# Kernel tuning notes

Measured on AMD Instinct MI355X. Metric: run time of the kernel, lower is better.

Reference implementation:

```python
import jax, jax.numpy as jnp
import numpy as np

B = 4096      # batch (tokens)
D_IN = 1024   # input_size_expert
D_HID = 4096  # hidden_size_expert
D_OUT = 1024  # output_size
E = 8         # num_experts


def setup_inputs() -> dict:
    key = jax.random.key(0)
    ks = jax.random.split(key, 9)
    s = lambda fan_in: 1.0 / np.sqrt(fan_in)
    x_expert = jax.random.normal(ks[0], (B, D_IN), dtype=jnp.float32)
    # per-expert weights stacked on leading E axis
    W1 = jax.random.uniform(ks[1], (E, D_IN, D_HID), jnp.float32, -s(D_IN), s(D_IN))
    b1 = jax.random.uniform(ks[2], (E, D_HID), jnp.float32, -s(D_IN), s(D_IN))
    W2 = jax.random.uniform(ks[3], (E, D_HID, D_OUT), jnp.float32, -s(D_HID), s(D_HID))
    b2 = jax.random.uniform(ks[4], (E, D_OUT), jnp.float32, -s(D_HID), s(D_HID))
    # gating network (input_size_gating = input_size_expert, hidden_size_gating = hidden_size_expert)
    Wg1 = jax.random.uniform(ks[5], (D_IN, D_HID), jnp.float32, -s(D_IN), s(D_IN))
    bg1 = jax.random.uniform(ks[6], (D_HID,), jnp.float32, -s(D_IN), s(D_IN))
    Wg2 = jax.random.uniform(ks[7], (D_HID, E), jnp.float32, -s(D_HID), s(D_HID))
    bg2 = jax.random.uniform(ks[8], (E,), jnp.float32, -s(D_HID), s(D_HID))
    return {"x_expert": x_expert, "W1": W1, "b1": b1, "W2": W2, "b2": b2,
            "Wg1": Wg1, "bg1": bg1, "Wg2": Wg2, "bg2": bg2}


def reference(x_expert, W1, b1, W2, b2, Wg1, bg1, Wg2, bg2):
    # gating: MLP + softmax over experts -> [B, E]
    g = jax.nn.relu(x_expert @ Wg1 + bg1)
    gate = jax.nn.softmax(g @ Wg2 + bg2, axis=1)
    # all experts as one batched GEMM: [B, E, D_HID]
    h = jax.nn.relu(jnp.einsum('bi,eih->beh', x_expert, W1) + b1)
    expert_out = jnp.einsum('beh,eho->beo', h, W2) + b2  # [B, E, D_OUT]
    # gate-weighted sum over experts
    return jnp.einsum('be,beo->bo', gate, expert_out)
```

## Files before the change

### kernel.cpp

```cpp
#include <hip/hip_runtime.h>
#include <stdint.h>

typedef __bf16 bf16;
typedef __attribute__((ext_vector_type(8))) __bf16 bf16x8;
typedef __attribute__((ext_vector_type(4))) float f32x4;
typedef unsigned short u16;
typedef unsigned int u32;

#define B_TOK 4096
#define D_IN  1024
#define D_HID 4096
#define D_OUT 1024
#define NE    8
#define KTOT  (NE * D_HID)

__device__ __forceinline__ u16 f2bf(float f) {
  u32 u = __float_as_uint(f);
  return (u16)((u + 0x7FFFu + ((u >> 16) & 1u)) >> 16);
}
__device__ __forceinline__ u32 pack2(float a, float b) {
  return (u32)f2bf(a) | ((u32)f2bf(b) << 16);
}

__global__ __launch_bounds__(256) void cvt_bf16_kernel(const float* __restrict__ in,
                                                       u32* __restrict__ out, long n) {
  long i = ((long)blockIdx.x * 256 + threadIdx.x) * 8;
  if (i >= n) return;
  const float4* pf = (const float4*)(in + i);
  float4 f0 = pf[0], f1 = pf[1];
  uint4 o = make_uint4(pack2(f0.x, f0.y), pack2(f0.z, f0.w),
                       pack2(f1.x, f1.y), pack2(f1.z, f1.w));
  *(uint4*)(out + i / 2) = o;
}

__global__ __launch_bounds__(256) void transpose_bf16_kernel(const float* __restrict__ in,
                                                             u16* __restrict__ out,
                                                             int R, int C) {
  __shared__ u16 tileT[64][68];
  const size_t bo = (size_t)blockIdx.z * R * C;
  const int c0 = blockIdx.x * 64, r0 = blockIdx.y * 64;
  const int tid = threadIdx.x;
  const int lr = tid >> 4;
  const int lc = (tid & 15) * 4;
#pragma unroll
  for (int p = 0; p < 4; ++p) {
    const int r = p * 16 + lr;
    const float4 v = *(const float4*)(in + bo + (size_t)(r0 + r) * C + c0 + lc);
    tileT[lc + 0][r] = f2bf(v.x);
    tileT[lc + 1][r] = f2bf(v.y);
    tileT[lc + 2][r] = f2bf(v.z);
    tileT[lc + 3][r] = f2bf(v.w);
  }
  __syncthreads();
  const int oc  = tid >> 3;
  const int och = (tid & 7) * 8;
#pragma unroll
  for (int p = 0; p < 2; ++p) {
    const int c = p * 32 + oc;
    bf16x8 v = *(const bf16x8*)(&tileT[c][och]);
    *(bf16x8*)(out + bo + (size_t)(c0 + c) * R + r0 + och) = v;
  }
}

template<int MODE>
__global__ __launch_bounds__(256, 4) void gemm_mfma(
    const bf16* __restrict__ A,
    const bf16* __restrict__ Bt,
    const float* __restrict__ bias,
    const float* __restrict__ gate,
    void* __restrict__ Cptr,
    int K, long ldB, long kOffB, long ldC, int kIters, int eArg)
{
  __shared__ __align__(16) bf16 smem[2 * 128 * 64];
  bf16* As = smem;
  bf16* Bs = smem + 128 * 64;

  const int tid  = threadIdx.x;
  const int wave = tid >> 6;
  const int lane = tid & 63;
  const int quad = lane >> 4;
  const int l16  = lane & 15;

  const int m0 = blockIdx.x * 128;
  const int n0 = blockIdx.y * 128;

  int expert = 0;
  long cColOff = 0;
  const bf16* Bp = Bt;
  const float* biasP = bias;
  if (MODE == 1) {
    if (gridDim.z > 1) { expert = blockIdx.z; cColOff = (long)expert * D_HID; }
    else               { expert = eArg; }
    Bp = Bt + (size_t)expert * D_HID * (size_t)ldB;
    biasP = bias + (size_t)expert * D_HID;
  }
  const long kBase = (MODE == 2) ? (long)blockIdx.z * kIters * 64 : 0;

  const int sRow = lane >> 3;
  const int sCol = ((lane & 7) ^ sRow) * 8;

  f32x4 acc[4][4];
#pragma unroll
  for (int i = 0; i < 4; ++i)
#pragma unroll
    for (int j = 0; j < 4; ++j)
      acc[i][j] = (f32x4){0.f, 0.f, 0.f, 0.f};

  const int wr = (wave >> 1) * 64;
  const int wc = (wave & 1) * 64;

  const bf16* aBase = A  + (size_t)(m0 + wave * 32 + sRow) * K   + kBase + sCol;
  const bf16* bBase = Bp + (size_t)(n0 + wave * 32 + sRow) * ldB + kOffB + kBase + sCol;
  bf16* asDst = As + (wave * 32) * 64;
  bf16* bsDst = Bs + (wave * 32) * 64;

  for (int kk = 0; kk < kIters; ++kk) {
    const long ko = (long)kk * 64;
#pragma unroll
    for (int s = 0; s < 4; ++s) {
      __builtin_amdgcn_global_load_lds(
          (__attribute__((address_space(1))) void*)(aBase + (size_t)(s * 8) * K + ko),
          (__attribute__((address_space(3))) void*)(asDst + s * 8 * 64), 16, 0, 0);
      __builtin_amdgcn_global_load_lds(
          (__attribute__((address_space(1))) void*)(bBase + (size_t)(s * 8) * ldB + ko),
          (__attribute__((address_space(3))) void*)(bsDst + s * 8 * 64), 16, 0, 0);
    }
    __syncthreads();
#pragma unroll
    for (int t = 0; t < 2; ++t) {
      bf16x8 af[4], bfv[4];
      const int sw = (((t << 2) + quad) ^ (l16 & 7)) << 3;
#pragma unroll
      for (int i = 0; i < 4; ++i) {
        af[i]  = *(const bf16x8*)(As + (wr + i * 16 + l16) * 64 + sw);
        bfv[i] = *(const bf16x8*)(Bs + (wc + i * 16 + l16) * 64 + sw);
      }
#pragma unroll
      for (int i = 0; i < 4; ++i)
#pragma unroll
        for (int j = 0; j < 4; ++j)
          acc[i][j] = __builtin_amdgcn_mfma_f32_16x16x32_bf16(af[i], bfv[j], acc[i][j], 0, 0, 0);
    }
    __syncthreads();
  }

  if (MODE <= 1) {
    const int SL = 72;
    u16* slab = (u16*)smem + wave * (16 * SL);
    u16* C = (u16*)Cptr;
    float bv[4];
#pragma unroll
    for (int j = 0; j < 4; ++j) bv[j] = biasP[n0 + wc + j * 16 + l16];
#pragma unroll
    for (int i = 0; i < 4; ++i) {
#pragma unroll
      for (int r = 0; r < 4; ++r) {
        const int lrow = quad * 4 + r;
        float sc = 1.0f;
        if (MODE == 1) sc = gate[(size_t)(m0 + wr + i * 16 + lrow) * NE + expert];
#pragma unroll
        for (int j = 0; j < 4; ++j) {
          float v = fmaxf(acc[i][j][r] + bv[j], 0.0f) * sc;
          slab[lrow * SL + j * 16 + l16] = f2bf(v);
        }
      }
      const int rrow = lane & 15;
      const int c0c  = lane >> 4;
      bf16x8 v0 = *(const bf16x8*)(slab + rrow * SL + c0c * 8);
      bf16x8 v1 = *(const bf16x8*)(slab + rrow * SL + (c0c + 4) * 8);
      u16* orow = C + (size_t)(m0 + wr + i * 16 + rrow) * ldC + cColOff + n0 + wc;
      *(bf16x8*)(orow + c0c * 8)       = v0;
      *(bf16x8*)(orow + (c0c + 4) * 8) = v1;
    }
  } else {
    float* C = (float*)Cptr;
#pragma unroll
    for (int i = 0; i < 4; ++i) {
#pragma unroll
      for (int r = 0; r < 4; ++r) {
        const int row = m0 + wr + i * 16 + quad * 4 + r;
        float* crow = C + (size_t)row * ldC + n0 + wc + l16;
#pragma unroll
        for (int j = 0; j < 4; ++j)
          atomicAdd(crow + j * 16, acc[i][j][r]);
      }
    }
  }
}

__global__ __launch_bounds__(256) void gate_softmax_kernel(const bf16* __restrict__ g,
                                                           const float* __restrict__ Wg2,
                                                           const float* __restrict__ bg2,
                                                           float* __restrict__ gate) {
  const int wave = threadIdx.x >> 6, lane = threadIdx.x & 63;
  const int row = blockIdx.x * 4 + wave;
  const bf16* gr = g + (size_t)row * D_HID;
  float acc[NE];
#pragma unroll
  for (int e = 0; e < NE; ++e) acc[e] = 0.f;
  for (int k = lane; k < D_HID; k += 64) {
    const float gv = (float)gr[k];
    const float* w = Wg2 + (size_t)k * NE;
#pragma unroll
    for (int e = 0; e < NE; ++e) acc[e] += gv * w[e];
  }
#pragma unroll
  for (int e = 0; e < NE; ++e) {
    float v = acc[e];
#pragma unroll
    for (int off = 32; off > 0; off >>= 1) v += __shfl_down(v, off);
    acc[e] = v;
  }
  if (lane == 0) {
    float mx = -3.4e38f;
#pragma unroll
    for (int e = 0; e < NE; ++e) { acc[e] += bg2[e]; mx = fmaxf(mx, acc[e]); }
    float s = 0.f;
#pragma unroll
    for (int e = 0; e < NE; ++e) { acc[e] = __expf(acc[e] - mx); s += acc[e]; }
    const float inv = 1.f / s;
#pragma unroll
    for (int e = 0; e < NE; ++e) gate[(size_t)row * NE + e] = acc[e] * inv;
  }
}

__global__ __launch_bounds__(256) void gate_bias_kernel(const float* __restrict__ gate,
                                                        const float* __restrict__ b2,
                                                        float* __restrict__ out) {
  const int idx = blockIdx.x * 256 + threadIdx.x;
  const int b = idx >> 8;
  const int o = (idx & 255) * 4;
  float4 v = {0.f, 0.f, 0.f, 0.f};
#pragma unroll
  for (int e = 0; e < NE; ++e) {
    const float gv = gate[(size_t)b * NE + e];
    const float4 bb = *(const float4*)(b2 + (size_t)e * D_OUT + o);
    v.x += gv * bb.x; v.y += gv * bb.y; v.z += gv * bb.z; v.w += gv * bb.w;
  }
  *(float4*)(out + (size_t)b * D_OUT + o) = v;
}

extern "C" void kernel_launch(void* const* d_in, const int* in_sizes, int n_in,
                              void* d_out, int out_size, void* d_ws, size_t ws_size,
                              hipStream_t stream) {
  const float* x   = (const float*)d_in[0];
  const float* W1  = (const float*)d_in[1];
  const float* b1  = (const float*)d_in[2];
  const float* W2  = (const float*)d_in[3];
  const float* b2  = (const float*)d_in[4];
  const float* Wg1 = (const float*)d_in[5];
  const float* bg1 = (const float*)d_in[6];
  const float* Wg2 = (const float*)d_in[7];
  const float* bg2 = (const float*)d_in[8];
  float* out = (float*)d_out;

  char* p = (char*)d_ws;
  bf16* xb   = (bf16*)p; p += (size_t)B_TOK * D_IN * 2;
  bf16* Wg1t = (bf16*)p; p += (size_t)D_HID * D_IN * 2;
  bf16* W1t  = (bf16*)p; p += (size_t)NE * D_HID * D_IN * 2;
  bf16* W2t  = (bf16*)p; p += (size_t)D_OUT * KTOT * 2;
  bf16* g    = (bf16*)p; p += (size_t)B_TOK * D_HID * 2;
  float* gate= (float*)p; p += (size_t)B_TOK * NE * 4;
  bf16* hs   = (bf16*)p;
  const size_t fixed = (size_t)(p - (char*)d_ws);
  const bool big = ws_size >= fixed + (size_t)B_TOK * KTOT * 2;

  cvt_bf16_kernel<<<(B_TOK * D_IN / 8 + 255) / 256, 256, 0, stream>>>(x, (u32*)xb, (long)B_TOK * D_IN);
  transpose_bf16_kernel<<<dim3(D_HID / 64, D_IN / 64, 1), 256, 0, stream>>>(Wg1, (u16*)Wg1t, D_IN, D_HID);
  transpose_bf16_kernel<<<dim3(D_HID / 64, D_IN / 64, NE), 256, 0, stream>>>(W1, (u16*)W1t, D_IN, D_HID);
  transpose_bf16_kernel<<<dim3(D_OUT / 64, KTOT / 64, 1), 256, 0, stream>>>(W2, (u16*)W2t, KTOT, D_OUT);
  gemm_mfma<0><<<dim3(32, 32, 1), 256, 0, stream>>>(xb, Wg1t, bg1, nullptr, g,
                                                    D_IN, (long)D_IN, 0L, (long)D_HID, D_IN / 64, 0);
  gate_softmax_kernel<<<B_TOK / 4, 256, 0, stream>>>(g, Wg2, bg2, gate);
  gate_bias_kernel<<<B_TOK * D_OUT / 4 / 256, 256, 0, stream>>>(gate, b2, out);

  if (big) {
    gemm_mfma<1><<<dim3(32, 32, NE), 256, 0, stream>>>(xb, W1t, b1, gate, hs,
                                                       D_IN, (long)D_IN, 0L, (long)KTOT, D_IN / 64, 0);
    gemm_mfma<2><<<dim3(32, 8, 4), 256, 0, stream>>>(hs, W2t, nullptr, nullptr, out,
                                                     KTOT, (long)KTOT, 0L, (long)D_OUT, KTOT / 4 / 64, 0);
  } else {
    for (int e = 0; e < NE; ++e) {
      gemm_mfma<1><<<dim3(32, 32, 1), 256, 0, stream>>>(xb, W1t, b1, gate, hs,
                                                        D_IN, (long)D_IN, 0L, (long)D_HID, D_IN / 64, e);
      gemm_mfma<2><<<dim3(32, 8, 2), 256, 0, stream>>>(hs, W2t, nullptr, nullptr, out,
                                                       D_HID, (long)KTOT, (long)e * D_HID, (long)D_OUT,
                                                       D_HID / 2 / 64, e);
    }
  }
}
```

Measured before the change: 1.032 ms.

## Move GEMMs to 256x256 tiles with 8 waves and double-buffered LDS prefetch

Replaces the 128x128, 4-wave MFMA GEMM with a 256x256-tile, 512-thread kernel. It double-buffers LDS so that global_load_lds for the next K tile is issued while MFMAs run on the current one. The K step is split into four phases with explicit barriers, waitcnts, sched_barriers and setprio to interleave LDS reads with MFMA bursts. The goal is more data reuse per block and hidden load latency. The cost is twice the LDS (128 KB), more accumulators per wave and lower occupancy, plus fewer blocks per launch for the smaller grids.

```diff
diff --git a/kernel.cpp b/kernel.cpp
--- a/kernel.cpp
+++ b/kernel.cpp
@@ -63,7 +63,7 @@
 }
 
 template<int MODE>
-__global__ __launch_bounds__(256, 4) void gemm_mfma(
+__global__ __launch_bounds__(512, 2) void gemm_mfma256(
     const bf16* __restrict__ A,
     const bf16* __restrict__ Bt,
     const float* __restrict__ bias,
@@ -71,18 +71,18 @@
     void* __restrict__ Cptr,
     int K, long ldB, long kOffB, long ldC, int kIters, int eArg)
 {
-  __shared__ __align__(16) bf16 smem[2 * 128 * 64];
-  bf16* As = smem;
-  bf16* Bs = smem + 128 * 64;
+  __shared__ __align__(16) bf16 smem[65536];
 
   const int tid  = threadIdx.x;
   const int wave = tid >> 6;
   const int lane = tid & 63;
   const int quad = lane >> 4;
   const int l16  = lane & 15;
-
-  const int m0 = blockIdx.x * 128;
-  const int n0 = blockIdx.y * 128;
+  const int wr = (wave >> 2) * 128;
+  const int wc = (wave & 3) * 64;
+
+  const int m0 = blockIdx.x * 256;
+  const int n0 = blockIdx.y * 256;
 
   int expert = 0;
   long cColOff = 0;
@@ -94,55 +94,127 @@
     Bp = Bt + (size_t)expert * D_HID * (size_t)ldB;
     biasP = bias + (size_t)expert * D_HID;
   }
-  const long kBase = (MODE == 2) ? (long)blockIdx.z * kIters * 64 : 0;
+  const int nt = kIters;
+  const long kBase = (MODE == 2) ? (long)blockIdx.z * nt * 64 : 0;
 
   const int sRow = lane >> 3;
   const int sCol = ((lane & 7) ^ sRow) * 8;
 
-  f32x4 acc[4][4];
-#pragma unroll
-  for (int i = 0; i < 4; ++i)
+  const bf16* aSrc = A  + (size_t)(m0 + wave * 8 + sRow) * K   + kBase + sCol;
+  const bf16* bSrc = Bp + (size_t)(n0 + wave * 8 + sRow) * ldB + kOffB + kBase + sCol;
+  const int dOff = (wave * 8) * 64;
+
+  f32x4 acc[8][4];
+#pragma unroll
+  for (int i = 0; i < 8; ++i)
 #pragma unroll
     for (int j = 0; j < 4; ++j)
       acc[i][j] = (f32x4){0.f, 0.f, 0.f, 0.f};
 
-  const int wr = (wave >> 1) * 64;
-  const int wc = (wave & 1) * 64;
-
-  const bf16* aBase = A  + (size_t)(m0 + wave * 32 + sRow) * K   + kBase + sCol;
-  const bf16* bBase = Bp + (size_t)(n0 + wave * 32 + sRow) * ldB + kOffB + kBase + sCol;
-  bf16* asDst = As + (wave * 32) * 64;
-  bf16* bsDst = Bs + (wave * 32) * 64;
-
-  for (int kk = 0; kk < kIters; ++kk) {
-    const long ko = (long)kk * 64;
-#pragma unroll
-    for (int s = 0; s < 4; ++s) {
-      __builtin_amdgcn_global_load_lds(
-          (__attribute__((address_space(1))) void*)(aBase + (size_t)(s * 8) * K + ko),
-          (__attribute__((address_space(3))) void*)(asDst + s * 8 * 64), 16, 0, 0);
-      __builtin_amdgcn_global_load_lds(
-          (__attribute__((address_space(1))) void*)(bBase + (size_t)(s * 8) * ldB + ko),
-          (__attribute__((address_space(3))) void*)(bsDst + s * 8 * 64), 16, 0, 0);
+#define GLLA(tt, bb) do { \
+    bf16* dstA = smem + (bb) * 32768 + dOff; \
+    const bf16* srcA = aSrc + (size_t)(tt) * 64; \
+    for (int g = 0; g < 4; ++g) \
+      __builtin_amdgcn_global_load_lds( \
+          (__attribute__((address_space(1))) void*)(srcA + (size_t)g * 64 * K), \
+          (__attribute__((address_space(3))) void*)(dstA + g * 64 * 64), 16, 0, 0); \
+  } while (0)
+#define GLLB(tt, bb) do { \
+    bf16* dstB = smem + (bb) * 32768 + 16384 + dOff; \
+    const bf16* srcB = bSrc + (size_t)(tt) * 64; \
+    for (int g = 0; g < 4; ++g) \
+      __builtin_amdgcn_global_load_lds( \
+          (__attribute__((address_space(1))) void*)(srcB + (size_t)g * 64 * ldB), \
+          (__attribute__((address_space(3))) void*)(dstB + g * 64 * 64), 16, 0, 0); \
+  } while (0)
+
+  GLLA(0, 0);
+  GLLB(0, 0);
+
+  for (int t = 0; t < nt; ++t) {
+    const int b = t & 1;
+    const bf16* As_ = smem + b * 32768;
+    const bf16* Bs_ = As_ + 16384;
+    const int swA = ((quad) ^ (l16 & 7)) << 3;
+    const int swB = ((4 + quad) ^ (l16 & 7)) << 3;
+    bf16x8 bfr[4], af[4];
+
+    if (t + 1 < nt) {
+      GLLA(t + 1, b ^ 1);
+      asm volatile("s_waitcnt vmcnt(4)");
+    } else {
+      asm volatile("s_waitcnt vmcnt(0)");
     }
-    __syncthreads();
-#pragma unroll
-    for (int t = 0; t < 2; ++t) {
-      bf16x8 af[4], bfv[4];
-      const int sw = (((t << 2) + quad) ^ (l16 & 7)) << 3;
-#pragma unroll
-      for (int i = 0; i < 4; ++i) {
-        af[i]  = *(const bf16x8*)(As + (wr + i * 16 + l16) * 64 + sw);
-        bfv[i] = *(const bf16x8*)(Bs + (wc + i * 16 + l16) * 64 + sw);
-      }
-#pragma unroll
-      for (int i = 0; i < 4; ++i)
-#pragma unroll
-        for (int j = 0; j < 4; ++j)
-          acc[i][j] = __builtin_amdgcn_mfma_f32_16x16x32_bf16(af[i], bfv[j], acc[i][j], 0, 0, 0);
-    }
-    __syncthreads();
-  }
+    __builtin_amdgcn_s_barrier();
+    __builtin_amdgcn_sched_barrier(0);
+#pragma unroll
+    for (int j = 0; j < 4; ++j)
+      bfr[j] = *(const bf16x8*)(Bs_ + (wc + j * 16 + l16) * 64 + swA);
+#pragma unroll
+    for (int i = 0; i < 4; ++i)
+      af[i] = *(const bf16x8*)(As_ + (wr + i * 16 + l16) * 64 + swA);
+    asm volatile("s_waitcnt lgkmcnt(0)");
+    __builtin_amdgcn_sched_barrier(0);
+    __builtin_amdgcn_s_setprio(1);
+#pragma unroll
+    for (int i = 0; i < 4; ++i)
+#pragma unroll
+      for (int j = 0; j < 4; ++j)
+        acc[i][j] = __builtin_amdgcn_mfma_f32_16x16x32_bf16(af[i], bfr[j], acc[i][j], 0, 0, 0);
+    __builtin_amdgcn_s_setprio(0);
+    __builtin_amdgcn_s_barrier();
+
+#pragma unroll
+    for (int i = 0; i < 4; ++i)
+      af[i] = *(const bf16x8*)(As_ + (wr + 64 + i * 16 + l16) * 64 + swA);
+    if (t + 1 < nt) GLLB(t + 1, b ^ 1);
+    __builtin_amdgcn_s_barrier();
+    asm volatile("s_waitcnt lgkmcnt(0)");
+    __builtin_amdgcn_sched_barrier(0);
+    __builtin_amdgcn_s_setprio(1);
+#pragma unroll
+    for (int i = 0; i < 4; ++i)
+#pragma unroll
+      for (int j = 0; j < 4; ++j)
+        acc[4 + i][j] = __builtin_amdgcn_mfma_f32_16x16x32_bf16(af[i], bfr[j], acc[4 + i][j], 0, 0, 0);
+    __builtin_amdgcn_s_setprio(0);
+    __builtin_amdgcn_s_barrier();
+
+#pragma unroll
+    for (int j = 0; j < 4; ++j)
+      bfr[j] = *(const bf16x8*)(Bs_ + (wc + j * 16 + l16) * 64 + swB);
+#pragma unroll
+    for (int i = 0; i < 4; ++i)
+      af[i] = *(const bf16x8*)(As_ + (wr + i * 16 + l16) * 64 + swB);
+    __builtin_amdgcn_s_barrier();
+    asm volatile("s_waitcnt lgkmcnt(0)");
+    __builtin_amdgcn_sched_barrier(0);
+    __builtin_amdgcn_s_setprio(1);
+#pragma unroll
+    for (int i = 0; i < 4; ++i)
+#pragma unroll
+      for (int j = 0; j < 4; ++j)
+        acc[i][j] = __builtin_amdgcn_mfma_f32_16x16x32_bf16(af[i], bfr[j], acc[i][j], 0, 0, 0);
+    __builtin_amdgcn_s_setprio(0);
+    __builtin_amdgcn_s_barrier();
+
+#pragma unroll
+    for (int i = 0; i < 4; ++i)
+      af[i] = *(const bf16x8*)(As_ + (wr + 64 + i * 16 + l16) * 64 + swB);
+    __builtin_amdgcn_s_barrier();
+    asm volatile("s_waitcnt lgkmcnt(0)");
+    __builtin_amdgcn_sched_barrier(0);
+    __builtin_amdgcn_s_setprio(1);
+#pragma unroll
+    for (int i = 0; i < 4; ++i)
+#pragma unroll
+      for (int j = 0; j < 4; ++j)
+        acc[4 + i][j] = __builtin_amdgcn_mfma_f32_16x16x32_bf16(af[i], bfr[j], acc[4 + i][j], 0, 0, 0);
+    __builtin_amdgcn_s_setprio(0);
+    __builtin_amdgcn_s_barrier();
+  }
+#undef GLLA
+#undef GLLB
 
   if (MODE <= 1) {
     const int SL = 72;
@@ -152,7 +224,7 @@
 #pragma unroll
     for (int j = 0; j < 4; ++j) bv[j] = biasP[n0 + wc + j * 16 + l16];
 #pragma unroll
-    for (int i = 0; i < 4; ++i) {
+    for (int i = 0; i < 8; ++i) {
 #pragma unroll
       for (int r = 0; r < 4; ++r) {
         const int lrow = quad * 4 + r;
@@ -175,7 +247,7 @@
   } else {
     float* C = (float*)Cptr;
 #pragma unroll
-    for (int i = 0; i < 4; ++i) {
+    for (int i = 0; i < 8; ++i) {
 #pragma unroll
       for (int r = 0; r < 4; ++r) {
         const int row = m0 + wr + i * 16 + quad * 4 + r;
@@ -269,23 +341,23 @@
   transpose_bf16_kernel<<<dim3(D_HID / 64, D_IN / 64, 1), 256, 0, stream>>>(Wg1, (u16*)Wg1t, D_IN, D_HID);
   transpose_bf16_kernel<<<dim3(D_HID / 64, D_IN / 64, NE), 256, 0, stream>>>(W1, (u16*)W1t, D_IN, D_HID);
   transpose_bf16_kernel<<<dim3(D_OUT / 64, KTOT / 64, 1), 256, 0, stream>>>(W2, (u16*)W2t, KTOT, D_OUT);
-  gemm_mfma<0><<<dim3(32, 32, 1), 256, 0, stream>>>(xb, Wg1t, bg1, nullptr, g,
-                                                    D_IN, (long)D_IN, 0L, (long)D_HID, D_IN / 64, 0);
+  gemm_mfma256<0><<<dim3(16, 16, 1), 512, 0, stream>>>(xb, Wg1t, bg1, nullptr, g,
+                                                       D_IN, (long)D_IN, 0L, (long)D_HID, D_IN / 64, 0);
   gate_softmax_kernel<<<B_TOK / 4, 256, 0, stream>>>(g, Wg2, bg2, gate);
   gate_bias_kernel<<<B_TOK * D_OUT / 4 / 256, 256, 0, stream>>>(gate, b2, out);
 
   if (big) {
-    gemm_mfma<1><<<dim3(32, 32, NE), 256, 0, stream>>>(xb, W1t, b1, gate, hs,
-                                                       D_IN, (long)D_IN, 0L, (long)KTOT, D_IN / 64, 0);
-    gemm_mfma<2><<<dim3(32, 8, 4), 256, 0, stream>>>(hs, W2t, nullptr, nullptr, out,
-                                                     KTOT, (long)KTOT, 0L, (long)D_OUT, KTOT / 4 / 64, 0);
+    gemm_mfma256<1><<<dim3(16, 16, NE), 512, 0, stream>>>(xb, W1t, b1, gate, hs,
+                                                          D_IN, (long)D_IN, 0L, (long)KTOT, D_IN / 64, 0);
+    gemm_mfma256<2><<<dim3(16, 4, 4), 512, 0, stream>>>(hs, W2t, nullptr, nullptr, out,
+                                                        KTOT, (long)KTOT, 0L, (long)D_OUT, KTOT / 4 / 64, 0);
   } else {
     for (int e = 0; e < NE; ++e) {
-      gemm_mfma<1><<<dim3(32, 32, 1), 256, 0, stream>>>(xb, W1t, b1, gate, hs,
-                                                        D_IN, (long)D_IN, 0L, (long)D_HID, D_IN / 64, e);
-      gemm_mfma<2><<<dim3(32, 8, 2), 256, 0, stream>>>(hs, W2t, nullptr, nullptr, out,
-                                                       D_HID, (long)KTOT, (long)e * D_HID, (long)D_OUT,
-                                                       D_HID / 2 / 64, e);
+      gemm_mfma256<1><<<dim3(16, 16, 1), 512, 0, stream>>>(xb, W1t, b1, gate, hs,
+                                                           D_IN, (long)D_IN, 0L, (long)D_HID, D_IN / 64, e);
+      gemm_mfma256<2><<<dim3(16, 4, 2), 512, 0, stream>>>(hs, W2t, nullptr, nullptr, out,
+                                                          D_HID, (long)KTOT, (long)e * D_HID, (long)D_OUT,
+                                                          D_HID / 2 / 64, e);
     }
   }
 }
```

After: 958.4 us. 7.1% less time.

## Rewrite MFMA GEMM as 256x256 tile, 512-thread kernel with 4-stage LDS pipeline

Applied to the files above, without the earlier changes.

Replaces the 128x128 single-buffered GEMM with a 256x256 tile kernel using 8 waves, each computing a 128x64 sub-tile. K tiles are 32 wide and move through a 4-deep LDS ring via global_load_lds, with loads issued three tiles ahead and explicit vmcnt waits, barriers and setprio around the MFMA bursts. Workgroup IDs are remapped so consecutive tiles are spread across the eight XCDs. The aim is to hide global-memory latency and raise arithmetic intensity per tile. The cost is more registers and LDS, and fewer workgroups, which hurts the small gating and split-K launches.

```diff
diff --git a/kernel.cpp b/kernel.cpp
--- a/kernel.cpp
+++ b/kernel.cpp
@@ -13,6 +13,9 @@
 #define D_OUT 1024
 #define NE    8
 #define KTOT  (NE * D_HID)
+
+#define AS1 __attribute__((address_space(1)))
+#define AS3 __attribute__((address_space(3)))
 
 __device__ __forceinline__ u16 f2bf(float f) {
   u32 u = __float_as_uint(f);
@@ -63,7 +66,7 @@
 }
 
 template<int MODE>
-__global__ __launch_bounds__(256, 4) void gemm_mfma(
+__global__ __launch_bounds__(512, 2) void gemm_mfma256(
     const bf16* __restrict__ A,
     const bf16* __restrict__ Bt,
     const float* __restrict__ bias,
@@ -71,78 +74,125 @@
     void* __restrict__ Cptr,
     int K, long ldB, long kOffB, long ldC, int kIters, int eArg)
 {
-  __shared__ __align__(16) bf16 smem[2 * 128 * 64];
-  bf16* As = smem;
-  bf16* Bs = smem + 128 * 64;
+  __shared__ __align__(16) bf16 smem[65536];
 
   const int tid  = threadIdx.x;
   const int wave = tid >> 6;
   const int lane = tid & 63;
   const int quad = lane >> 4;
   const int l16  = lane & 15;
-
-  const int m0 = blockIdx.x * 128;
-  const int n0 = blockIdx.y * 128;
+  const int wr = (wave >> 2) * 128;
+  const int wc = (wave & 3) * 64;
+
+  const int gx = gridDim.x, gy = gridDim.y;
+  const int nwg = gx * gy * gridDim.z;
+  const int orig = blockIdx.x + gx * (blockIdx.y + gy * blockIdx.z);
+  const int cid = (orig & 7) * (nwg >> 3) + (orig >> 3);
+  const int bx = cid % gx;
+  const int rest = cid / gx;
+  const int by = rest % gy;
+  const int bz = rest / gy;
+
+  const int m0 = bx * 256;
+  const int n0 = by * 256;
 
   int expert = 0;
   long cColOff = 0;
   const bf16* Bp = Bt;
   const float* biasP = bias;
   if (MODE == 1) {
-    if (gridDim.z > 1) { expert = blockIdx.z; cColOff = (long)expert * D_HID; }
+    if (gridDim.z > 1) { expert = bz; cColOff = (long)expert * D_HID; }
     else               { expert = eArg; }
     Bp = Bt + (size_t)expert * D_HID * (size_t)ldB;
     biasP = bias + (size_t)expert * D_HID;
   }
-  const long kBase = (MODE == 2) ? (long)blockIdx.z * kIters * 64 : 0;
-
-  const int sRow = lane >> 3;
-  const int sCol = ((lane & 7) ^ sRow) * 8;
-
-  f32x4 acc[4][4];
-#pragma unroll
-  for (int i = 0; i < 4; ++i)
+  const int nt = kIters;
+  const long kBase = (MODE == 2) ? (long)bz * nt * 32 : 0;
+
+  const int sRow = lane >> 2;
+  const int sCol = ((lane & 3) ^ ((lane >> 3) & 3)) * 8;
+
+  const bf16* aSrc = A  + (size_t)(m0 + wave * 32 + sRow) * K   + kBase + sCol;
+  const bf16* bSrc = Bp + (size_t)(n0 + wave * 32 + sRow) * ldB + kOffB + kBase + sCol;
+
+  const int xorv = (quad ^ ((l16 >> 1) & 3)) * 8;
+  int aOff[8], bOff[4];
+#pragma unroll
+  for (int i = 0; i < 8; ++i) aOff[i] = (wr + i * 16 + l16) * 32 + xorv;
+#pragma unroll
+  for (int j = 0; j < 4; ++j) bOff[j] = (wc + j * 16 + l16) * 32 + xorv;
+
+  f32x4 acc[8][4];
+#pragma unroll
+  for (int i = 0; i < 8; ++i)
 #pragma unroll
     for (int j = 0; j < 4; ++j)
       acc[i][j] = (f32x4){0.f, 0.f, 0.f, 0.f};
 
-  const int wr = (wave >> 1) * 64;
-  const int wc = (wave & 1) * 64;
-
-  const bf16* aBase = A  + (size_t)(m0 + wave * 32 + sRow) * K   + kBase + sCol;
-  const bf16* bBase = Bp + (size_t)(n0 + wave * 32 + sRow) * ldB + kOffB + kBase + sCol;
-  bf16* asDst = As + (wave * 32) * 64;
-  bf16* bsDst = Bs + (wave * 32) * 64;
-
-  for (int kk = 0; kk < kIters; ++kk) {
-    const long ko = (long)kk * 64;
-#pragma unroll
-    for (int s = 0; s < 4; ++s) {
-      __builtin_amdgcn_global_load_lds(
-          (__attribute__((address_space(1))) void*)(aBase + (size_t)(s * 8) * K + ko),
-          (__attribute__((address_space(3))) void*)(asDst + s * 8 * 64), 16, 0, 0);
-      __builtin_amdgcn_global_load_lds(
-          (__attribute__((address_space(1))) void*)(bBase + (size_t)(s * 8) * ldB + ko),
-          (__attribute__((address_space(3))) void*)(bsDst + s * 8 * 64), 16, 0, 0);
-    }
-    __syncthreads();
-#pragma unroll
-    for (int t = 0; t < 2; ++t) {
-      bf16x8 af[4], bfv[4];
-      const int sw = (((t << 2) + quad) ^ (l16 & 7)) << 3;
-#pragma unroll
-      for (int i = 0; i < 4; ++i) {
-        af[i]  = *(const bf16x8*)(As + (wr + i * 16 + l16) * 64 + sw);
-        bfv[i] = *(const bf16x8*)(Bs + (wc + i * 16 + l16) * 64 + sw);
-      }
-#pragma unroll
-      for (int i = 0; i < 4; ++i)
-#pragma unroll
-        for (int j = 0; j < 4; ++j)
-          acc[i][j] = __builtin_amdgcn_mfma_f32_16x16x32_bf16(af[i], bfv[j], acc[i][j], 0, 0, 0);
-    }
-    __syncthreads();
-  }
+#define GLLA(tt, bb) do { \
+    bf16* d_ = smem + (bb) * 16384 + wave * 1024; \
+    const bf16* s_ = aSrc + (size_t)(tt) * 32; \
+    __builtin_amdgcn_global_load_lds((AS1 void*)(s_), (AS3 void*)(d_), 16, 0, 0); \
+    __builtin_amdgcn_global_load_lds((AS1 void*)(s_ + (size_t)16 * K), (AS3 void*)(d_ + 512), 16, 0, 0); \
+  } while (0)
+#define GLLB(tt, bb) do { \
+    bf16* d_ = smem + (bb) * 16384 + 8192 + wave * 1024; \
+    const bf16* s_ = bSrc + (size_t)(tt) * 32; \
+    __builtin_amdgcn_global_load_lds((AS1 void*)(s_), (AS3 void*)(d_), 16, 0, 0); \
+    __builtin_amdgcn_global_load_lds((AS1 void*)(s_ + (size_t)16 * ldB), (AS3 void*)(d_ + 512), 16, 0, 0); \
+  } while (0)
+
+#define TILE_BODY(T, VMW, ISS) do { \
+    const bf16* Ab_ = smem + ((T) & 3) * 16384; \
+    const bf16* Bb_ = Ab_ + 8192; \
+    bf16x8 af_[4], bf_[4]; \
+    if (ISS) GLLA((T) + 3, ((T) + 3) & 3); \
+    asm volatile("s_waitcnt vmcnt(" #VMW ")"); \
+    __builtin_amdgcn_s_barrier(); \
+    __builtin_amdgcn_sched_barrier(0); \
+    _Pragma("unroll") \
+    for (int j_ = 0; j_ < 4; ++j_) bf_[j_] = *(const bf16x8*)(Bb_ + bOff[j_]); \
+    _Pragma("unroll") \
+    for (int i_ = 0; i_ < 4; ++i_) af_[i_] = *(const bf16x8*)(Ab_ + aOff[i_]); \
+    asm volatile("s_waitcnt lgkmcnt(0)"); \
+    __builtin_amdgcn_sched_barrier(0); \
+    __builtin_amdgcn_s_setprio(1); \
+    _Pragma("unroll") \
+    for (int i_ = 0; i_ < 4; ++i_) \
+      _Pragma("unroll") \
+      for (int j_ = 0; j_ < 4; ++j_) \
+        acc[i_][j_] = __builtin_amdgcn_mfma_f32_16x16x32_bf16(af_[i_], bf_[j_], acc[i_][j_], 0, 0, 0); \
+    __builtin_amdgcn_s_setprio(0); \
+    __builtin_amdgcn_s_barrier(); \
+    _Pragma("unroll") \
+    for (int i_ = 0; i_ < 4; ++i_) af_[i_] = *(const bf16x8*)(Ab_ + aOff[4 + i_]); \
+    if (ISS) GLLB((T) + 3, ((T) + 3) & 3); \
+    __builtin_amdgcn_s_barrier(); \
+    asm volatile("s_waitcnt lgkmcnt(0)"); \
+    __builtin_amdgcn_sched_barrier(0); \
+    __builtin_amdgcn_s_setprio(1); \
+    _Pragma("unroll") \
+    for (int i_ = 0; i_ < 4; ++i_) \
+      _Pragma("unroll") \
+      for (int j_ = 0; j_ < 4; ++j_) \
+        acc[4 + i_][j_] = __builtin_amdgcn_mfma_f32_16x16x32_bf16(af_[i_], bf_[j_], acc[4 + i_][j_], 0, 0, 0); \
+    __builtin_amdgcn_s_setprio(0); \
+    __builtin_amdgcn_s_barrier(); \
+  } while (0)
+
+  GLLA(0, 0); GLLB(0, 0);
+  GLLA(1, 1); GLLB(1, 1);
+  GLLA(2, 2); GLLB(2, 2);
+
+  int t = 0;
+  for (; t < nt - 3; ++t) TILE_BODY(t, 10, 1);
+  TILE_BODY(t, 8, 0); ++t;
+  TILE_BODY(t, 4, 0); ++t;
+  TILE_BODY(t, 0, 0);
+
+#undef GLLA
+#undef GLLB
+#undef TILE_BODY
 
   if (MODE <= 1) {
     const int SL = 72;
@@ -152,7 +202,7 @@
 #pragma unroll
     for (int j = 0; j < 4; ++j) bv[j] = biasP[n0 + wc + j * 16 + l16];
 #pragma unroll
-    for (int i = 0; i < 4; ++i) {
+    for (int i = 0; i < 8; ++i) {
 #pragma unroll
       for (int r = 0; r < 4; ++r) {
         const int lrow = quad * 4 + r;
@@ -175,7 +225,7 @@
   } else {
     float* C = (float*)Cptr;
 #pragma unroll
-    for (int i = 0; i < 4; ++i) {
+    for (int i = 0; i < 8; ++i) {
 #pragma unroll
       for (int r = 0; r < 4; ++r) {
         const int row = m0 + wr + i * 16 + quad * 4 + r;
@@ -269,23 +319,23 @@
   transpose_bf16_kernel<<<dim3(D_HID / 64, D_IN / 64, 1), 256, 0, stream>>>(Wg1, (u16*)Wg1t, D_IN, D_HID);
   transpose_bf16_kernel<<<dim3(D_HID / 64, D_IN / 64, NE), 256, 0, stream>>>(W1, (u16*)W1t, D_IN, D_HID);
   transpose_bf16_kernel<<<dim3(D_OUT / 64, KTOT / 64, 1), 256, 0, stream>>>(W2, (u16*)W2t, KTOT, D_OUT);
-  gemm_mfma<0><<<dim3(32, 32, 1), 256, 0, stream>>>(xb, Wg1t, bg1, nullptr, g,
-                                                    D_IN, (long)D_IN, 0L, (long)D_HID, D_IN / 64, 0);
+  gemm_mfma256<0><<<dim3(16, 16, 1), 512, 0, stream>>>(xb, Wg1t, bg1, nullptr, g,
+                                                       D_IN, (long)D_IN, 0L, (long)D_HID, D_IN / 32, 0);
   gate_softmax_kernel<<<B_TOK / 4, 256, 0, stream>>>(g, Wg2, bg2, gate);
   gate_bias_kernel<<<B_TOK * D_OUT / 4 / 256, 256, 0, stream>>>(gate, b2, out);
 
   if (big) {
-    gemm_mfma<1><<<dim3(32, 32, NE), 256, 0, stream>>>(xb, W1t, b1, gate, hs,
-                                                       D_IN, (long)D_IN, 0L, (long)KTOT, D_IN / 64, 0);
-    gemm_mfma<2><<<dim3(32, 8, 4), 256, 0, stream>>>(hs, W2t, nullptr, nullptr, out,
-                                                     KTOT, (long)KTOT, 0L, (long)D_OUT, KTOT / 4 / 64, 0);
+    gemm_mfma256<1><<<dim3(16, 16, NE), 512, 0, stream>>>(xb, W1t, b1, gate, hs,
+                                                          D_IN, (long)D_IN, 0L, (long)KTOT, D_IN / 32, 0);
+    gemm_mfma256<2><<<dim3(16, 4, 4), 512, 0, stream>>>(hs, W2t, nullptr, nullptr, out,
+                                                        KTOT, (long)KTOT, 0L, (long)D_OUT, KTOT / 4 / 32, 0);
   } else {
     for (int e = 0; e < NE; ++e) {
-      gemm_mfma<1><<<dim3(32, 32, 1), 256, 0, stream>>>(xb, W1t, b1, gate, hs,
-                                                        D_IN, (long)D_IN, 0L, (long)D_HID, D_IN / 64, e);
-      gemm_mfma<2><<<dim3(32, 8, 2), 256, 0, stream>>>(hs, W2t, nullptr, nullptr, out,
-                                                       D_HID, (long)KTOT, (long)e * D_HID, (long)D_OUT,
-                                                       D_HID / 2 / 64, e);
+      gemm_mfma256<1><<<dim3(16, 16, 1), 512, 0, stream>>>(xb, W1t, b1, gate, hs,
+                                                           D_IN, (long)D_IN, 0L, (long)D_HID, D_IN / 32, e);
+      gemm_mfma256<2><<<dim3(16, 4, 2), 512, 0, stream>>>(hs, W2t, nullptr, nullptr, out,
+                                                          D_HID, (long)KTOT, (long)e * D_HID, (long)D_OUT,
+                                                          D_HID / 2 / 32, e);
     }
   }
 }
```

Result: slower. 1.087 ms (+5.3%).

## Switch GEMMs to 256x256 tiles with 8 waves and double-buffered LDS loads

Applied to the files above, without the earlier changes.

Replaces the 128x128, 4-wave GEMM with a 256x256-tile, 512-thread kernel. Each wave now computes a 128x64 sub-tile with 8x4 MFMA accumulators. LDS is double-buffered so the next K tile's global-to-LDS load overlaps the current tile's MFMAs, with one barrier per iteration, and s_setprio raises wave priority around the MFMA block. The aim is more data reuse per byte loaded and less sync stall. The cost is much higher register and LDS use (128KB smem), fewer blocks in flight, and a smaller grid for the gating GEMM.

```diff
diff --git a/kernel.cpp b/kernel.cpp
--- a/kernel.cpp
+++ b/kernel.cpp
@@ -13,6 +13,9 @@
 #define D_OUT 1024
 #define NE    8
 #define KTOT  (NE * D_HID)
+
+#define AS1 __attribute__((address_space(1)))
+#define AS3 __attribute__((address_space(3)))
 
 __device__ __forceinline__ u16 f2bf(float f) {
   u32 u = __float_as_uint(f);
@@ -63,7 +66,7 @@
 }
 
 template<int MODE>
-__global__ __launch_bounds__(256, 4) void gemm_mfma(
+__global__ __launch_bounds__(512, 2) void gemm_mfma256(
     const bf16* __restrict__ A,
     const bf16* __restrict__ Bt,
     const float* __restrict__ bias,
@@ -71,18 +74,18 @@
     void* __restrict__ Cptr,
     int K, long ldB, long kOffB, long ldC, int kIters, int eArg)
 {
-  __shared__ __align__(16) bf16 smem[2 * 128 * 64];
-  bf16* As = smem;
-  bf16* Bs = smem + 128 * 64;
+  __shared__ __align__(16) bf16 smem[65536];
 
   const int tid  = threadIdx.x;
   const int wave = tid >> 6;
   const int lane = tid & 63;
   const int quad = lane >> 4;
   const int l16  = lane & 15;
-
-  const int m0 = blockIdx.x * 128;
-  const int n0 = blockIdx.y * 128;
+  const int wr = (wave >> 2) * 128;
+  const int wc = (wave & 3) * 64;
+
+  const int m0 = blockIdx.x * 256;
+  const int n0 = blockIdx.y * 256;
 
   int expert = 0;
   long cColOff = 0;
@@ -94,55 +97,65 @@
     Bp = Bt + (size_t)expert * D_HID * (size_t)ldB;
     biasP = bias + (size_t)expert * D_HID;
   }
-  const long kBase = (MODE == 2) ? (long)blockIdx.z * kIters * 64 : 0;
+  const int nt = kIters;
+  const long kBase = (MODE == 2) ? (long)blockIdx.z * nt * 64 : 0;
 
   const int sRow = lane >> 3;
   const int sCol = ((lane & 7) ^ sRow) * 8;
 
-  f32x4 acc[4][4];
-#pragma unroll
-  for (int i = 0; i < 4; ++i)
+  const bf16* aSrc = A  + (size_t)(m0 + wave * 8 + sRow) * K   + kBase + sCol;
+  const bf16* bSrc = Bp + (size_t)(n0 + wave * 8 + sRow) * ldB + kOffB + kBase + sCol;
+  const int dOff = (wave * 8) * 64;
+
+  f32x4 acc[8][4];
+#pragma unroll
+  for (int i = 0; i < 8; ++i)
 #pragma unroll
     for (int j = 0; j < 4; ++j)
       acc[i][j] = (f32x4){0.f, 0.f, 0.f, 0.f};
 
-  const int wr = (wave >> 1) * 64;
-  const int wc = (wave & 1) * 64;
-
-  const bf16* aBase = A  + (size_t)(m0 + wave * 32 + sRow) * K   + kBase + sCol;
-  const bf16* bBase = Bp + (size_t)(n0 + wave * 32 + sRow) * ldB + kOffB + kBase + sCol;
-  bf16* asDst = As + (wave * 32) * 64;
-  bf16* bsDst = Bs + (wave * 32) * 64;
-
-  for (int kk = 0; kk < kIters; ++kk) {
-    const long ko = (long)kk * 64;
-#pragma unroll
-    for (int s = 0; s < 4; ++s) {
-      __builtin_amdgcn_global_load_lds(
-          (__attribute__((address_space(1))) void*)(aBase + (size_t)(s * 8) * K + ko),
-          (__attribute__((address_space(3))) void*)(asDst + s * 8 * 64), 16, 0, 0);
-      __builtin_amdgcn_global_load_lds(
-          (__attribute__((address_space(1))) void*)(bBase + (size_t)(s * 8) * ldB + ko),
-          (__attribute__((address_space(3))) void*)(bsDst + s * 8 * 64), 16, 0, 0);
+#define GLL(tt, bb) do { \
+    bf16* dstA = smem + (bb) * 32768 + dOff; \
+    bf16* dstB = dstA + 16384; \
+    const bf16* srcA = aSrc + (size_t)(tt) * 64; \
+    const bf16* srcB = bSrc + (size_t)(tt) * 64; \
+    _Pragma("unroll") \
+    for (int g_ = 0; g_ < 4; ++g_) { \
+      __builtin_amdgcn_global_load_lds((AS1 void*)(srcA + (size_t)g_ * 64 * K), \
+                                       (AS3 void*)(dstA + g_ * 64 * 64), 16, 0, 0); \
+      __builtin_amdgcn_global_load_lds((AS1 void*)(srcB + (size_t)g_ * 64 * ldB), \
+                                       (AS3 void*)(dstB + g_ * 64 * 64), 16, 0, 0); \
+    } \
+  } while (0)
+
+  GLL(0, 0);
+
+  for (int t = 0; t < nt; ++t) {
+    const bf16* Ab = smem + (t & 1) * 32768;
+    const bf16* Bb = Ab + 16384;
+    asm volatile("s_waitcnt vmcnt(0)" ::: "memory");
+    __builtin_amdgcn_s_barrier();
+    if (t + 1 < nt) GLL(t + 1, (t + 1) & 1);
+#pragma unroll
+    for (int kh = 0; kh < 2; ++kh) {
+      const int sw = (((kh << 2) + quad) ^ (l16 & 7)) << 3;
+      bf16x8 bv[4], av[8];
+#pragma unroll
+      for (int j = 0; j < 4; ++j)
+        bv[j] = *(const bf16x8*)(Bb + (wc + j * 16 + l16) * 64 + sw);
+#pragma unroll
+      for (int i = 0; i < 8; ++i)
+        av[i] = *(const bf16x8*)(Ab + (wr + i * 16 + l16) * 64 + sw);
+      __builtin_amdgcn_s_setprio(1);
+#pragma unroll
+      for (int i = 0; i < 8; ++i)
+#pragma unroll
+        for (int j = 0; j < 4; ++j)
+          acc[i][j] = __builtin_amdgcn_mfma_f32_16x16x32_bf16(av[i], bv[j], acc[i][j], 0, 0, 0);
+      __builtin_amdgcn_s_setprio(0);
     }
-    __syncthreads();
-#pragma unroll
-    for (int t = 0; t < 2; ++t) {
-      bf16x8 af[4], bfv[4];
-      const int sw = (((t << 2) + quad) ^ (l16 & 7)) << 3;
-#pragma unroll
-      for (int i = 0; i < 4; ++i) {
-        af[i]  = *(const bf16x8*)(As + (wr + i * 16 + l16) * 64 + sw);
-        bfv[i] = *(const bf16x8*)(Bs + (wc + i * 16 + l16) * 64 + sw);
-      }
-#pragma unroll
-      for (int i = 0; i < 4; ++i)
-#pragma unroll
-        for (int j = 0; j < 4; ++j)
-          acc[i][j] = __builtin_amdgcn_mfma_f32_16x16x32_bf16(af[i], bfv[j], acc[i][j], 0, 0, 0);
-    }
-    __syncthreads();
-  }
+  }
+#undef GLL
 
   if (MODE <= 1) {
     const int SL = 72;
@@ -152,7 +165,7 @@
 #pragma unroll
     for (int j = 0; j < 4; ++j) bv[j] = biasP[n0 + wc + j * 16 + l16];
 #pragma unroll
-    for (int i = 0; i < 4; ++i) {
+    for (int i = 0; i < 8; ++i) {
 #pragma unroll
       for (int r = 0; r < 4; ++r) {
         const int lrow = quad * 4 + r;
@@ -175,7 +188,7 @@
   } else {
     float* C = (float*)Cptr;
 #pragma unroll
-    for (int i = 0; i < 4; ++i) {
+    for (int i = 0; i < 8; ++i) {
 #pragma unroll
       for (int r = 0; r < 4; ++r) {
         const int row = m0 + wr + i * 16 + quad * 4 + r;
@@ -269,23 +282,23 @@
   transpose_bf16_kernel<<<dim3(D_HID / 64, D_IN / 64, 1), 256, 0, stream>>>(Wg1, (u16*)Wg1t, D_IN, D_HID);
   transpose_bf16_kernel<<<dim3(D_HID / 64, D_IN / 64, NE), 256, 0, stream>>>(W1, (u16*)W1t, D_IN, D_HID);
   transpose_bf16_kernel<<<dim3(D_OUT / 64, KTOT / 64, 1), 256, 0, stream>>>(W2, (u16*)W2t, KTOT, D_OUT);
-  gemm_mfma<0><<<dim3(32, 32, 1), 256, 0, stream>>>(xb, Wg1t, bg1, nullptr, g,
-                                                    D_IN, (long)D_IN, 0L, (long)D_HID, D_IN / 64, 0);
+  gemm_mfma256<0><<<dim3(16, 16, 1), 512, 0, stream>>>(xb, Wg1t, bg1, nullptr, g,
+                                                       D_IN, (long)D_IN, 0L, (long)D_HID, D_IN / 64, 0);
   gate_softmax_kernel<<<B_TOK / 4, 256, 0, stream>>>(g, Wg2, bg2, gate);
   gate_bias_kernel<<<B_TOK * D_OUT / 4 / 256, 256, 0, stream>>>(gate, b2, out);
 
   if (big) {
-    gemm_mfma<1><<<dim3(32, 32, NE), 256, 0, stream>>>(xb, W1t, b1, gate, hs,
-                                                       D_IN, (long)D_IN, 0L, (long)KTOT, D_IN / 64, 0);
-    gemm_mfma<2><<<dim3(32, 8, 4), 256, 0, stream>>>(hs, W2t, nullptr, nullptr, out,
-                                                     KTOT, (long)KTOT, 0L, (long)D_OUT, KTOT / 4 / 64, 0);
+    gemm_mfma256<1><<<dim3(16, 16, NE), 512, 0, stream>>>(xb, W1t, b1, gate, hs,
+                                                          D_IN, (long)D_IN, 0L, (long)KTOT, D_IN / 64, 0);
+    gemm_mfma256<2><<<dim3(16, 4, 8), 512, 0, stream>>>(hs, W2t, nullptr, nullptr, out,
+                                                        KTOT, (long)KTOT, 0L, (long)D_OUT, KTOT / 8 / 64, 0);
   } else {
     for (int e = 0; e < NE; ++e) {
-      gemm_mfma<1><<<dim3(32, 32, 1), 256, 0, stream>>>(xb, W1t, b1, gate, hs,
-                                                        D_IN, (long)D_IN, 0L, (long)D_HID, D_IN / 64, e);
-      gemm_mfma<2><<<dim3(32, 8, 2), 256, 0, stream>>>(hs, W2t, nullptr, nullptr, out,
-                                                       D_HID, (long)KTOT, (long)e * D_HID, (long)D_OUT,
-                                                       D_HID / 2 / 64, e);
+      gemm_mfma256<1><<<dim3(16, 16, 1), 512, 0, stream>>>(xb, W1t, b1, gate, hs,
+                                                           D_IN, (long)D_IN, 0L, (long)D_HID, D_IN / 64, e);
+      gemm_mfma256<2><<<dim3(16, 4, 2), 512, 0, stream>>>(hs, W2t, nullptr, nullptr, out,
+                                                          D_HID, (long)KTOT, (long)e * D_HID, (long)D_OUT,
+                                                          D_HID / 2 / 64, e);
     }
   }
 }
```

Measured after the change: 1.006 ms. 2.6% less time.
